# Optimization experiments

Measured on AMD Instinct MI355X. Metric: run time of the kernel, lower is better.

Reference implementation:

```python
import jax, jax.numpy as jnp
import numpy as np

B, C1, C2, H, L, D, NC = 32, 256, 256, 64, 40, 768, 8
SIGMA_W = 0.1
EMB = (D + NC * 2) // 2  # 392


def _conv(x, w, scale, shift, pad):
    # ultralytics-style Conv: conv2d(bias=False) + eval-mode BN (folded into per-channel
    # scale/shift) + SiLU activation
    y = jax.lax.conv_general_dilated(x, w, (1, 1), [(pad, pad), (pad, pad)],
                                     dimension_numbers=('NCHW', 'OIHW', 'NCHW'))
    y = y * scale[None, :, None, None] + shift[None, :, None, None]
    return y * jax.nn.sigmoid(y)  # SiLU


def _l2norm(x, eps=1e-12):
    n = jnp.sqrt(jnp.sum(x * x, axis=1, keepdims=True))
    return x / jnp.maximum(n, eps)


def setup_inputs() -> dict:
    key = jax.random.key(0)
    ks = jax.random.split(key, 20)
    img = jax.random.normal(ks[0], (B, C1, H, H), jnp.float32)
    flang = jax.random.normal(ks[1], (B, L, D), jnp.float32)
    # contiguous valid mask with >=3 tokens (CLS + >=1 word + SEP)
    lens = jax.random.randint(ks[2], (B,), 3, L + 1)
    word_mask = (jnp.arange(L)[None, :] < lens[:, None]).astype(jnp.int32)
    p = lambda k, s: jax.random.normal(k, s, jnp.float32) * 0.02
    return {
        'img': img, 'flang': flang, 'word_mask': word_mask,
        'w_visu': p(ks[3], (C2, C1, 1, 1)), 's_visu': jnp.ones((C2,)), 'b_visu': jnp.zeros((C2,)),
        'w_g': p(ks[4], (NC, NC, 1, 1)), 's_g': jnp.ones((NC,)), 'b_g': jnp.zeros((NC,)),
        'w_b': p(ks[5], (NC, NC, 1, 1)), 's_b': jnp.ones((NC,)), 'b_b': jnp.zeros((NC,)),
        'W1': p(ks[6], (EMB, D)), 'b1': jnp.zeros((EMB,)),
        'W2': p(ks[7], (2 * NC, EMB)), 'b2': jnp.zeros((2 * NC,)),
        'w_f1': p(ks[8], (C1, C1, 1, 1)), 's_f1': jnp.ones((C1,)), 'b_f1': jnp.zeros((C1,)),
        'w_f2': p(ks[9], (C1, C1, 3, 3)), 's_f2': jnp.ones((C1,)), 'b_f2': jnp.zeros((C1,)),
        'w_f3': p(ks[10], (C2, C1, 1, 1)), 'bias_f3': jnp.zeros((C2,)),
        'add_weight': jnp.zeros((), jnp.float32),
    }


def reference(img, flang, word_mask, w_visu, s_visu, b_visu, w_g, s_g, b_g,
              w_b, s_b, b_b, W1, b1, W2, b2, w_f1, s_f1, b_f1, w_f2, s_f2, b_f2,
              w_f3, bias_f3, add_weight):
    height = img.shape[2]
    # mapping_visu: Conv 1x1 + BN + SiLU, then tanh
    map_visu = jnp.tanh(_conv(img, w_visu, s_visu, b_visu, 0))  # [B,C2,H,H]

    # vectorized get_avg_flang: mean over selected tokens excluding first and last selected
    m = word_mask.astype(jnp.int32)
    csum = jnp.cumsum(m, axis=1)                     # [B,L]
    total = csum[:, -1:]
    inner = ((m == 1) & (csum > 1) & (csum < total)).astype(flang.dtype)  # [B,L]
    cnt = jnp.sum(inner, axis=1, keepdims=True)
    flang_avg = jnp.sum(flang * inner[:, :, None], axis=1) / cnt  # [B,D]

    # mapping_lang: two stacked Linears (no activation between), then sigmoid
    h = flang_avg @ W1.T + b1
    map_flang = jax.nn.sigmoid(h @ W2.T + b2)        # [B,2*NC]
    maps = map_flang.reshape(-1, NC, 2)

    sigma = SIGMA_W * height
    yc = (maps[:, :, 0] * height).astype(jnp.int32)[:, :, None, None]
    xc = (maps[:, :, 1] * height).astype(jnp.int32)[:, :, None, None]
    gy, gx = jnp.meshgrid(jnp.arange(height), jnp.arange(height), indexing='ij')
    gy = gy[None, None]; gx = gx[None, None]
    d2 = ((gy - yc) ** 2 + (gx - xc) ** 2).astype(jnp.float32)
    weights = jnp.exp(-d2 / (2.0 * sigma ** 2))      # [B,NC,H,H]

    gamma = jnp.tanh(_conv(weights, w_g, s_g, b_g, 0))
    beta = jnp.tanh(_conv(weights, w_b, s_b, b_b, 0))
    g = jnp.mean(gamma, axis=1, keepdims=True)       # [B,1,H,H]
    b = jnp.max(beta, axis=1, keepdims=True)         # [B,1,H,H]

    v_film = _l2norm(g * map_visu + b)               # [B,C2,H,H]
    # mapping_fusion: Conv1x1 -> Conv3x3 -> plain Conv2d 1x1 with bias
    v = _conv(v_film, w_f1, s_f1, b_f1, 0)
    v = _conv(v, w_f2, s_f2, b_f2, 1)
    v_film = jax.lax.conv_general_dilated(v, w_f3, (1, 1), [(0, 0), (0, 0)],
                                          dimension_numbers=('NCHW', 'OIHW', 'NCHW'))
    v_film = v_film + bias_f3[None, :, None, None]

    add_w = jnp.tanh(add_weight)
    v_add = (1.0 + add_w) * img + (1.0 - add_w) * v_film
    return _l2norm(v_add)
```

## Files before the change

kernel.cpp:

```cpp
#include <hip/hip_runtime.h>
#include <hip/hip_bf16.h>

#define B_   32
#define C_   256
#define HH   64
#define P_   4096
#define L_   40
#define D_   768
#define NC_  8
#define EMB_ 392
#define CP_  (C_*P_)
#define LOS  264

typedef __attribute__((ext_vector_type(8))) short bf16x8;
typedef __attribute__((ext_vector_type(4))) float f32x4;
typedef unsigned short u16;

static __device__ __forceinline__ float siluf(float y) {
    return y / (1.f + expf(-y));
}
static __device__ __forceinline__ u16 f2b(float f) {
    __hip_bfloat16 h = __float2bfloat16(f);
    return *reinterpret_cast<u16*>(&h);
}
static __device__ __forceinline__ float b2f(u16 u) {
    unsigned v = ((unsigned)u) << 16;
    return __int_as_float((int)v);
}

typedef __attribute__((address_space(1))) const unsigned int g_u32;
typedef __attribute__((address_space(3))) unsigned int l_u32;
static __device__ __forceinline__ void gl_lds(const u16* g, short* l) {
    __builtin_amdgcn_global_load_lds((g_u32*)g, (l_u32*)l, 16, 0, 0);
}
#define VMCNT6() asm volatile("s_waitcnt vmcnt(6)" ::: "memory")
#define VMCNT0() asm volatile("s_waitcnt vmcnt(0)" ::: "memory")
#define RBAR()  do { __builtin_amdgcn_s_barrier(); __builtin_amdgcn_sched_barrier(0); } while (0)

__global__ __launch_bounds__(256) void k_prep(
    const float* __restrict__ wv, const float* __restrict__ wf1,
    const float* __restrict__ wf3, const float* __restrict__ wf2,
    u16* __restrict__ WV, u16* __restrict__ WF1,
    u16* __restrict__ WF3, u16* __restrict__ WF2, u16* __restrict__ zblk)
{
    int i = blockIdx.x * 256 + threadIdx.x;
    int oc = i >> 8, ic = i & 255;
    WV[i]  = f2b(wv[i]);
    WF1[i] = f2b(wf1[i]);
    WF3[i] = f2b(wf3[i]);
#pragma unroll
    for (int tap = 0; tap < 9; ++tap)
        WF2[oc * 2304 + tap * 256 + ic] = f2b(wf2[oc * 2304 + ic * 9 + tap]);
    if (blockIdx.x == 0 && threadIdx.x < 16) zblk[threadIdx.x] = 0;
}

__global__ __launch_bounds__(256) void k_imgT(
    const float* __restrict__ img, u16* __restrict__ imgT)
{
    int b = blockIdx.z, pix0 = blockIdx.x * 32, ic0 = blockIdx.y * 32;
    int t = threadIdx.x;
    __shared__ float T[32][33];
    int ic = t >> 3, ps = (t & 7) * 4;
    f32x4 v = *(const f32x4*)&img[((size_t)b * C_ + ic0 + ic) * P_ + pix0 + ps];
    T[ic][ps] = v[0]; T[ic][ps + 1] = v[1]; T[ic][ps + 2] = v[2]; T[ic][ps + 3] = v[3];
    __syncthreads();
    int px = t >> 3, sg = (t & 7) * 4;
    u16 o0 = f2b(T[sg + 0][px]), o1 = f2b(T[sg + 1][px]);
    u16 o2 = f2b(T[sg + 2][px]), o3 = f2b(T[sg + 3][px]);
    uint2 val;
    val.x = (unsigned)o0 | ((unsigned)o1 << 16);
    val.y = (unsigned)o2 | ((unsigned)o3 << 16);
    *(uint2*)(imgT + ((size_t)b * P_ + pix0 + px) * C_ + ic0 + sg) = val;
}

__global__ __launch_bounds__(256) void k_lang(
    const float* __restrict__ flang, const int* __restrict__ wmask,
    const float* __restrict__ W1, const float* __restrict__ b1,
    const float* __restrict__ W2, const float* __restrict__ b2,
    int* __restrict__ centers)
{
    int b = blockIdx.x, tid = threadIdx.x;
    __shared__ float inner[L_];
    __shared__ float cnt_s;
    __shared__ float favg[D_];
    __shared__ float hbuf[EMB_];
    __shared__ float mfs[16];

    if (tid == 0) {
        int total = 0;
        for (int l = 0; l < L_; ++l) total += wmask[b * L_ + l];
        int c = 0, cntv = 0;
        for (int l = 0; l < L_; ++l) {
            int m = wmask[b * L_ + l];
            c += m;
            float f = (m == 1 && c > 1 && c < total) ? 1.f : 0.f;
            inner[l] = f;
            cntv += (f != 0.f);
        }
        cnt_s = (float)cntv;
    }
    __syncthreads();
    float cinv = 1.f / cnt_s;
    for (int d = tid; d < D_; d += 256) {
        float s = 0.f;
        for (int l = 0; l < L_; ++l)
            s += flang[((size_t)b * L_ + l) * D_ + d] * inner[l];
        favg[d] = s * cinv;
    }
    __syncthreads();
    for (int e = tid; e < EMB_; e += 256) {
        float s = b1[e];
        const float* w = W1 + (size_t)e * D_;
        for (int d = 0; d < D_; ++d) s += w[d] * favg[d];
        hbuf[e] = s;
    }
    __syncthreads();
    if (tid < 16) {
        float s = b2[tid];
        const float* w = W2 + tid * EMB_;
        for (int d = 0; d < EMB_; ++d) s += w[d] * hbuf[d];
        mfs[tid] = 1.f / (1.f + expf(-s));
    }
    __syncthreads();
    if (tid < NC_) {
        centers[b * (NC_ * 2) + tid * 2 + 0] = (int)(mfs[tid * 2 + 0] * (float)HH);
        centers[b * (NC_ * 2) + tid * 2 + 1] = (int)(mfs[tid * 2 + 1] * (float)HH);
    }
}

__global__ __launch_bounds__(256) void k_gb(
    const int* __restrict__ centers,
    const float* __restrict__ wg, const float* __restrict__ sg, const float* __restrict__ bg,
    const float* __restrict__ wb, const float* __restrict__ sb, const float* __restrict__ bb,
    float* __restrict__ gmap, float* __restrict__ bmap)
{
    int idx = blockIdx.x * 256 + threadIdx.x;
    int b = idx >> 12;
    int p = idx & 4095;
    int gy = p >> 6, gx = p & 63;

    float w[NC_];
#pragma unroll
    for (int nc = 0; nc < NC_; ++nc) {
        int yc = centers[b * (NC_ * 2) + nc * 2 + 0];
        int xc = centers[b * (NC_ * 2) + nc * 2 + 1];
        int dy = gy - yc, dx = gx - xc;
        w[nc] = expf(-(float)(dy * dy + dx * dx) / 81.92f);
    }
    float gsum = 0.f, bmx = -1e30f;
#pragma unroll
    for (int c = 0; c < NC_; ++c) {
        float ag = 0.f, ab = 0.f;
#pragma unroll
        for (int ic = 0; ic < NC_; ++ic) {
            ag += wg[c * NC_ + ic] * w[ic];
            ab += wb[c * NC_ + ic] * w[ic];
        }
        gsum += tanhf(siluf(sg[c] * ag + bg[c]));
        bmx = fmaxf(bmx, tanhf(siluf(sb[c] * ab + bb[c])));
    }
    gmap[idx] = gsum * (1.f / (float)NC_);
    bmap[idx] = bmx;
}

static __device__ __forceinline__ void frag_load(const short* sA, const short* sW,
                                                 int l15, int qa, int w,
                                                 bf16x8 a[8], bf16x8 bb[4])
{
#pragma unroll
    for (int m = 0; m < 8; ++m)
        a[m] = *(const bf16x8*)&sA[(m * 16 + l15) * 32 + qa * 8];
#pragma unroll
    for (int n = 0; n < 4; ++n)
        bb[n] = *(const bf16x8*)&sW[(w * 64 + n * 16 + l15) * 32 + qa * 8];
}
static __device__ __forceinline__ void frag_compute(const bf16x8 a[8], const bf16x8 bb[4],
                                                    f32x4 acc[8][4])
{
#pragma unroll
    for (int m = 0; m < 8; ++m)
#pragma unroll
        for (int n = 0; n < 4; ++n)
            acc[m][n] = __builtin_amdgcn_mfma_f32_16x16x32_bf16(a[m], bb[n], acc[m][n], 0, 0, 0);
}

__global__ __launch_bounds__(256, 2) void k_visu(
    const u16* __restrict__ X, const u16* __restrict__ W,
    const float* __restrict__ s_visu, const float* __restrict__ b_visu,
    const float* __restrict__ gmap, const float* __restrict__ bmap,
    u16* __restrict__ Y)
{
    int b = blockIdx.y, p0 = blockIdx.x * 128, t = threadIdx.x;
    int lane = t & 63, w = t >> 6;
    int l15 = t & 15, q = (t >> 4) & 3;
    int qa = q ^ ((l15 >> 1) & 3);
    int lc = (lane & 3) ^ ((lane >> 3) & 3);
    int lp = lane >> 2;
    __shared__ __align__(16) short SM[128 * LOS];
    __shared__ float red[4][128];
    __shared__ float invs[128];
    const u16* Xb = X + (size_t)b * CP_;

    f32x4 acc[8][4];
#pragma unroll
    for (int m = 0; m < 8; ++m)
#pragma unroll
        for (int n = 0; n < 4; ++n) acc[m][n] = (f32x4)0.f;

    auto stage = [&](int s, int buf) {
        int k0 = s * 32;
        short* bA = SM + buf * 12288;
        short* bW = bA + 4096;
#pragma unroll
        for (int i = 0; i < 2; ++i) {
            int pr = (w * 2 + i) * 16 + lp;
            gl_lds(Xb + (size_t)(p0 + pr) * C_ + k0 + lc * 8, bA + (w * 2 + i) * 512);
        }
#pragma unroll
        for (int j = 0; j < 4; ++j) {
            int oc = (w * 4 + j) * 16 + lp;
            gl_lds(W + (size_t)oc * 256 + k0 + lc * 8, bW + (w * 4 + j) * 512);
        }
    };

    stage(0, 0);
    VMCNT0();
    __syncthreads();
    for (int s = 0; s < 8; ++s) {
        int cur = s & 1;
        bf16x8 a[8], bb[4];
        frag_load(SM + cur * 12288, SM + cur * 12288 + 4096, l15, qa, w, a, bb);
        if (s < 7) stage(s + 1, cur ^ 1);
        frag_compute(a, bb, acc);
        VMCNT0();
        __syncthreads();
    }

    float sc[4], sh[4];
#pragma unroll
    for (int n = 0; n < 4; ++n) {
        int oc = w * 64 + n * 16 + l15;
        sc[n] = s_visu[oc]; sh[n] = b_visu[oc];
    }
    short* LO = SM;
#pragma unroll
    for (int m = 0; m < 8; ++m) {
        f32x4 gv = *(const f32x4*)&gmap[(size_t)b * P_ + p0 + m * 16 + q * 4];
        f32x4 bm = *(const f32x4*)&bmap[(size_t)b * P_ + p0 + m * 16 + q * 4];
        float ps[4] = {0.f, 0.f, 0.f, 0.f};
#pragma unroll
        for (int n = 0; n < 4; ++n)
#pragma unroll
            for (int r = 0; r < 4; ++r) {
                float y = sc[n] * acc[m][n][r] + sh[n];
                float v = gv[r] * tanhf(siluf(y)) + bm[r];
                ps[r] += v * v;
                LO[(m * 16 + q * 4 + r) * LOS + w * 64 + n * 16 + l15] = (short)f2b(v);
            }
#pragma unroll
        for (int r = 0; r < 4; ++r) {
            float p = ps[r];
            p += __shfl_xor(p, 1);
            p += __shfl_xor(p, 2);
            p += __shfl_xor(p, 4);
            p += __shfl_xor(p, 8);
            if (l15 == 0) red[w][m * 16 + q * 4 + r] = p;
        }
    }
    __syncthreads();
    if (t < 128) {
        float s = red[0][t] + red[1][t] + red[2][t] + red[3][t];
        invs[t] = 1.f / fmaxf(sqrtf(s), 1e-12f);
    }
    __syncthreads();

    u16* Yb = Y + (size_t)b * CP_ + (size_t)p0 * C_;
#pragma unroll
    for (int h = 0; h < 2; ++h) {
        int row = h * 64 + (t >> 2);
        float inv = invs[row];
        const short* sp = &LO[row * LOS];
        u16* dp = Yb + (size_t)row * C_;
#pragma unroll
        for (int u = 0; u < 8; ++u) {
            int c = (t & 3) * 8 + u * 32;
            uint4 vv = *(const uint4*)(sp + c);
            const u16* e = (const u16*)&vv;
            uint4 o;
            u16* oe = (u16*)&o;
#pragma unroll
            for (int k = 0; k < 8; ++k) oe[k] = f2b(b2f(e[k]) * inv);
            *(uint4*)(dp + c) = o;
        }
    }
}

__global__ __launch_bounds__(256, 2) void k_f1(
    const u16* __restrict__ X, const u16* __restrict__ W,
    const float* __restrict__ scale, const float* __restrict__ shift,
    u16* __restrict__ Y)
{
    int b = blockIdx.y, p0 = blockIdx.x * 128, t = threadIdx.x;
    int lane = t & 63, w = t >> 6;
    int l15 = t & 15, q = (t >> 4) & 3;
    int qa = q ^ ((l15 >> 1) & 3);
    int lc = (lane & 3) ^ ((lane >> 3) & 3);
    int lp = lane >> 2;
    __shared__ __align__(16) short SM[128 * LOS];
    const u16* Xb = X + (size_t)b * CP_;

    f32x4 acc[8][4];
#pragma unroll
    for (int m = 0; m < 8; ++m)
#pragma unroll
        for (int n = 0; n < 4; ++n) acc[m][n] = (f32x4)0.f;

    auto stage = [&](int s, int buf) {
        int k0 = s * 32;
        short* bA = SM + buf * 12288;
        short* bW = bA + 4096;
#pragma unroll
        for (int i = 0; i < 2; ++i) {
            int pr = (w * 2 + i) * 16 + lp;
            gl_lds(Xb + (size_t)(p0 + pr) * C_ + k0 + lc * 8, bA + (w * 2 + i) * 512);
        }
#pragma unroll
        for (int j = 0; j < 4; ++j) {
            int oc = (w * 4 + j) * 16 + lp;
            gl_lds(W + (size_t)oc * 256 + k0 + lc * 8, bW + (w * 4 + j) * 512);
        }
    };

    stage(0, 0);
    VMCNT0();
    __syncthreads();
    for (int s = 0; s < 8; ++s) {
        int cur = s & 1;
        bf16x8 a[8], bb[4];
        frag_load(SM + cur * 12288, SM + cur * 12288 + 4096, l15, qa, w, a, bb);
        if (s < 7) stage(s + 1, cur ^ 1);
        frag_compute(a, bb, acc);
        VMCNT0();
        __syncthreads();
    }

    float sc[4], sh[4];
#pragma unroll
    for (int n = 0; n < 4; ++n) {
        int oc = w * 64 + n * 16 + l15;
        sc[n] = scale[oc]; sh[n] = shift[oc];
    }
    short* LO = SM;
#pragma unroll
    for (int m = 0; m < 8; ++m)
#pragma unroll
        for (int n = 0; n < 4; ++n)
#pragma unroll
            for (int r = 0; r < 4; ++r) {
                float v = siluf(sc[n] * acc[m][n][r] + sh[n]);
                LO[(m * 16 + q * 4 + r) * LOS + w * 64 + n * 16 + l15] = (short)f2b(v);
            }
    __syncthreads();

    u16* Yb = Y + (size_t)b * CP_ + (size_t)p0 * C_;
#pragma unroll
    for (int h = 0; h < 2; ++h) {
        int row = h * 64 + (t >> 2);
        const short* sp = &LO[row * LOS];
        u16* dp = Yb + (size_t)row * C_;
#pragma unroll
        for (int u = 0; u < 8; ++u) {
            int c = (t & 3) * 8 + u * 32;
            *(uint4*)(dp + c) = *(const uint4*)(sp + c);
        }
    }
}

__global__ __launch_bounds__(256, 2) void k_f2(
    const u16* __restrict__ X, const u16* __restrict__ W,
    const float* __restrict__ scale, const float* __restrict__ shift,
    const u16* __restrict__ zblk, u16* __restrict__ Y)
{
    int b = blockIdx.y, p0 = blockIdx.x * 128, t = threadIdx.x;
    int lane = t & 63, w = t >> 6;
    int l15 = t & 15, q = (t >> 4) & 3;
    int qa = q ^ ((l15 >> 1) & 3);
    int lc = (lane & 3) ^ ((lane >> 3) & 3);
    int lp = lane >> 2;
    __shared__ __align__(16) short SM[3 * 12288];
    const u16* Xb = X + (size_t)b * CP_;

    f32x4 acc[8][4];
#pragma unroll
    for (int m = 0; m < 8; ++m)
#pragma unroll
        for (int n = 0; n < 4; ++n) acc[m][n] = (f32x4)0.f;

    auto stage = [&](int s, int buf) {
        int k0 = s * 32;
        int tap = s >> 3;
        int icb = (s & 7) * 32;
        int dy = tap / 3 - 1, dx = tap - (tap / 3) * 3 - 1;
        short* bA = SM + buf * 12288;
        short* bW = bA + 4096;
#pragma unroll
        for (int i = 0; i < 2; ++i) {
            int pr = (w * 2 + i) * 16 + lp;
            int p = p0 + pr;
            int y = (p >> 6) + dy, x = (p & 63) + dx;
            const u16* gp = ((unsigned)y < (unsigned)HH && (unsigned)x < (unsigned)HH)
                ? Xb + (size_t)(y * HH + x) * C_ + icb + lc * 8
                : zblk;
            gl_lds(gp, bA + (w * 2 + i) * 512);
        }
#pragma unroll
        for (int j = 0; j < 4; ++j) {
            int oc = (w * 4 + j) * 16 + lp;
            gl_lds(W + (size_t)oc * 2304 + k0 + lc * 8, bW + (w * 4 + j) * 512);
        }
    };

    stage(0, 0);
    stage(1, 1);
    VMCNT6();
    RBAR();
    for (int s = 0; s < 72; ++s) {
        int cur = s % 3;
        bf16x8 a[8], bb[4];
        frag_load(SM + cur * 12288, SM + cur * 12288 + 4096, l15, qa, w, a, bb);
        if (s < 70) stage(s + 2, (s + 2) % 3);
        frag_compute(a, bb, acc);
        if (s < 70) { VMCNT6(); } else { VMCNT0(); }
        RBAR();
    }

    float sc[4], sh[4];
#pragma unroll
    for (int n = 0; n < 4; ++n) {
        int oc = w * 64 + n * 16 + l15;
        sc[n] = scale[oc]; sh[n] = shift[oc];
    }
    short* LO = SM;
#pragma unroll
    for (int m = 0; m < 8; ++m)
#pragma unroll
        for (int n = 0; n < 4; ++n)
#pragma unroll
            for (int r = 0; r < 4; ++r) {
                float v = siluf(sc[n] * acc[m][n][r] + sh[n]);
                LO[(m * 16 + q * 4 + r) * LOS + w * 64 + n * 16 + l15] = (short)f2b(v);
            }
    __syncthreads();

    u16* Yb = Y + (size_t)b * CP_ + (size_t)p0 * C_;
#pragma unroll
    for (int h = 0; h < 2; ++h) {
        int row = h * 64 + (t >> 2);
        const short* sp = &LO[row * LOS];
        u16* dp = Yb + (size_t)row * C_;
#pragma unroll
        for (int u = 0; u < 8; ++u) {
            int c = (t & 3) * 8 + u * 32;
            *(uint4*)(dp + c) = *(const uint4*)(sp + c);
        }
    }
}

__global__ __launch_bounds__(256, 2) void k_final(
    const u16* __restrict__ X, const u16* __restrict__ W,
    const float* __restrict__ bias_f3, const float* __restrict__ img,
    const float* __restrict__ add_w, float* __restrict__ out)
{
    int b = blockIdx.y, p0 = blockIdx.x * 128, t = threadIdx.x;
    int lane = t & 63, w = t >> 6;
    int l15 = t & 15, q = (t >> 4) & 3;
    int qa = q ^ ((l15 >> 1) & 3);
    int lc = (lane & 3) ^ ((lane >> 3) & 3);
    int lp = lane >> 2;
    __shared__ __align__(16) short SM[2 * 12288];
    __shared__ float red[4][128];
    __shared__ float invs[128];
    const u16* Xb = X + (size_t)b * CP_;

    f32x4 acc[8][4];
#pragma unroll
    for (int m = 0; m < 8; ++m)
#pragma unroll
        for (int n = 0; n < 4; ++n) acc[m][n] = (f32x4)0.f;

    auto stage = [&](int s, int buf) {
        int k0 = s * 32;
        short* bA = SM + buf * 12288;
        short* bW = bA + 4096;
#pragma unroll
        for (int i = 0; i < 2; ++i) {
            int pr = (w * 2 + i) * 16 + lp;
            gl_lds(Xb + (size_t)(p0 + pr) * C_ + k0 + lc * 8, bA + (w * 2 + i) * 512);
        }
#pragma unroll
        for (int j = 0; j < 4; ++j) {
            int oc = (w * 4 + j) * 16 + lp;
            gl_lds(W + (size_t)oc * 256 + k0 + lc * 8, bW + (w * 4 + j) * 512);
        }
    };

    stage(0, 0);
    VMCNT0();
    __syncthreads();
    for (int s = 0; s < 8; ++s) {
        int cur = s & 1;
        bf16x8 a[8], bb[4];
        frag_load(SM + cur * 12288, SM + cur * 12288 + 4096, l15, qa, w, a, bb);
        if (s < 7) stage(s + 1, cur ^ 1);
        frag_compute(a, bb, acc);
        VMCNT0();
        __syncthreads();
    }

    float aw = tanhf(add_w[0]);
    float c1 = 1.f + aw, c2 = 1.f - aw;
    float bf[4];
#pragma unroll
    for (int n = 0; n < 4; ++n) bf[n] = bias_f3[w * 64 + n * 16 + l15];

#pragma unroll
    for (int m = 0; m < 8; ++m) {
        float ps[4] = {0.f, 0.f, 0.f, 0.f};
#pragma unroll
        for (int n = 0; n < 4; ++n) {
            int oc = w * 64 + n * 16 + l15;
            f32x4 iv = *(const f32x4*)&img[((size_t)b * C_ + oc) * P_ + p0 + m * 16 + q * 4];
#pragma unroll
            for (int r = 0; r < 4; ++r) {
                float v = c1 * iv[r] + c2 * (acc[m][n][r] + bf[n]);
                acc[m][n][r] = v;
                ps[r] += v * v;
            }
        }
#pragma unroll
        for (int r = 0; r < 4; ++r) {
            float p = ps[r];
            p += __shfl_xor(p, 1);
            p += __shfl_xor(p, 2);
            p += __shfl_xor(p, 4);
            p += __shfl_xor(p, 8);
            if (l15 == 0) red[w][m * 16 + q * 4 + r] = p;
        }
    }
    __syncthreads();
    if (t < 128) {
        float s = red[0][t] + red[1][t] + red[2][t] + red[3][t];
        invs[t] = 1.f / fmaxf(sqrtf(s), 1e-12f);
    }
    __syncthreads();
#pragma unroll
    for (int m = 0; m < 8; ++m) {
        f32x4 iv = *(const f32x4*)&invs[m * 16 + q * 4];
#pragma unroll
        for (int n = 0; n < 4; ++n) {
            int oc = w * 64 + n * 16 + l15;
            f32x4 o;
#pragma unroll
            for (int r = 0; r < 4; ++r) o[r] = acc[m][n][r] * iv[r];
            *(f32x4*)&out[((size_t)b * C_ + oc) * P_ + p0 + m * 16 + q * 4] = o;
        }
    }
}

extern "C" void kernel_launch(void* const* d_in, const int* in_sizes, int n_in,
                              void* d_out, int out_size, void* d_ws, size_t ws_size,
                              hipStream_t stream)
{
    const float* img     = (const float*)d_in[0];
    const float* flang   = (const float*)d_in[1];
    const int*   wmask   = (const int*)d_in[2];
    const float* w_visu  = (const float*)d_in[3];
    const float* s_visu  = (const float*)d_in[4];
    const float* b_visu  = (const float*)d_in[5];
    const float* w_g     = (const float*)d_in[6];
    const float* s_g     = (const float*)d_in[7];
    const float* b_g     = (const float*)d_in[8];
    const float* w_b     = (const float*)d_in[9];
    const float* s_b     = (const float*)d_in[10];
    const float* b_b     = (const float*)d_in[11];
    const float* W1      = (const float*)d_in[12];
    const float* b1      = (const float*)d_in[13];
    const float* W2      = (const float*)d_in[14];
    const float* b2      = (const float*)d_in[15];
    const float* w_f1    = (const float*)d_in[16];
    const float* s_f1    = (const float*)d_in[17];
    const float* b_f1    = (const float*)d_in[18];
    const float* w_f2    = (const float*)d_in[19];
    const float* s_f2    = (const float*)d_in[20];
    const float* b_f2    = (const float*)d_in[21];
    const float* w_f3    = (const float*)d_in[22];
    const float* bias_f3 = (const float*)d_in[23];
    const float* add_w   = (const float*)d_in[24];

    float* out = (float*)d_out;

    u16* bigA = (u16*)d_ws;
    u16* bigB = bigA + (size_t)B_ * CP_;
    u16* WV   = bigB + (size_t)B_ * CP_;
    u16* WF1  = WV + 65536;
    u16* WF3  = WF1 + 65536;
    u16* WF2  = WF3 + 65536;
    float* gmap = (float*)(WF2 + 589824);
    float* bmap = gmap + (size_t)B_ * P_;
    int* centers = (int*)(bmap + (size_t)B_ * P_);
    u16* zblk = (u16*)(centers + 512);

    k_prep<<<256, 256, 0, stream>>>(w_visu, w_f1, w_f3, w_f2, WV, WF1, WF3, WF2, zblk);
    k_lang<<<B_, 256, 0, stream>>>(flang, wmask, W1, b1, W2, b2, centers);
    k_gb<<<(B_ * P_) / 256, 256, 0, stream>>>(centers, w_g, s_g, b_g, w_b, s_b, b_b, gmap, bmap);
    k_imgT<<<dim3(P_ / 32, C_ / 32, B_), 256, 0, stream>>>(img, bigB);
    k_visu<<<dim3(P_ / 128, B_), 256, 0, stream>>>(bigB, WV, s_visu, b_visu, gmap, bmap, bigA);
    k_f1<<<dim3(P_ / 128, B_), 256, 0, stream>>>(bigA, WF1, s_f1, b_f1, bigB);
    k_f2<<<dim3(P_ / 128, B_), 256, 0, stream>>>(bigB, WF2, s_f2, b_f2, zblk, bigA);
    k_final<<<dim3(P_ / 128, B_), 256, 0, stream>>>(bigA, WF3, bias_f3, img, add_w, out);
}
```

Baseline: 490.3 us.

## Fuse visual mapping conv and first fusion 1x1 conv into one kernel

Merges the visual 1x1 conv (with FiLM modulation and L2 normalisation) and the following 1x1 fusion conv into a single kernel. The normalised tile stays in a swizzled shared-memory buffer and feeds the second GEMM directly, with only the weights streamed. This removes one full bf16 activation write and read through global memory plus a kernel launch. The trade-off is that the second GEMM loads its weights without double buffering, adding a global-load wait each k-step. Output is written in place over the input buffer, which is safe because each block reads only its own rows.

```diff
diff --git a/kernel.cpp b/kernel.cpp
--- a/kernel.cpp
+++ b/kernel.cpp
@@ -27,6 +27,10 @@
     unsigned v = ((unsigned)u) << 16;
     return __int_as_float((int)v);
 }
+static __device__ __forceinline__ int swz(int row, int col) {
+    int ch = (col >> 3) ^ ((row & 7) << 2);
+    return row * 256 + ch * 8 + (col & 7);
+}
 
 typedef __attribute__((address_space(1))) const unsigned int g_u32;
 typedef __attribute__((address_space(3))) unsigned int l_u32;
@@ -184,10 +188,11 @@
             acc[m][n] = __builtin_amdgcn_mfma_f32_16x16x32_bf16(a[m], bb[n], acc[m][n], 0, 0, 0);
 }
 
-__global__ __launch_bounds__(256, 2) void k_visu(
-    const u16* __restrict__ X, const u16* __restrict__ W,
+__global__ __launch_bounds__(256, 2) void k_vf1(
+    const u16* __restrict__ X, const u16* __restrict__ WV, const u16* __restrict__ WF1,
     const float* __restrict__ s_visu, const float* __restrict__ b_visu,
     const float* __restrict__ gmap, const float* __restrict__ bmap,
+    const float* __restrict__ s_f1, const float* __restrict__ b_f1,
     u16* __restrict__ Y)
 {
     int b = blockIdx.y, p0 = blockIdx.x * 128, t = threadIdx.x;
@@ -196,9 +201,10 @@
     int qa = q ^ ((l15 >> 1) & 3);
     int lc = (lane & 3) ^ ((lane >> 3) & 3);
     int lp = lane >> 2;
-    __shared__ __align__(16) short SM[128 * LOS];
-    __shared__ float red[4][128];
-    __shared__ float invs[128];
+    __shared__ __align__(16) short LO[32768];
+    __shared__ __align__(16) short W2[8192];
+    float* red  = (float*)W2;
+    float* invs = (float*)(W2 + 1024);
     const u16* Xb = X + (size_t)b * CP_;
 
     f32x4 acc[8][4];
@@ -207,9 +213,9 @@
 #pragma unroll
         for (int n = 0; n < 4; ++n) acc[m][n] = (f32x4)0.f;
 
-    auto stage = [&](int s, int buf) {
+    auto stage1 = [&](int s, int buf) {
         int k0 = s * 32;
-        short* bA = SM + buf * 12288;
+        short* bA = LO + buf * 12288;
         short* bW = bA + 4096;
 #pragma unroll
         for (int i = 0; i < 2; ++i) {
@@ -219,159 +225,132 @@
 #pragma unroll
         for (int j = 0; j < 4; ++j) {
             int oc = (w * 4 + j) * 16 + lp;
-            gl_lds(W + (size_t)oc * 256 + k0 + lc * 8, bW + (w * 4 + j) * 512);
+            gl_lds(WV + (size_t)oc * 256 + k0 + lc * 8, bW + (w * 4 + j) * 512);
         }
     };
-
-    stage(0, 0);
+    stage1(0, 0);
     VMCNT0();
     __syncthreads();
     for (int s = 0; s < 8; ++s) {
         int cur = s & 1;
         bf16x8 a[8], bb[4];
-        frag_load(SM + cur * 12288, SM + cur * 12288 + 4096, l15, qa, w, a, bb);
-        if (s < 7) stage(s + 1, cur ^ 1);
+        frag_load(LO + cur * 12288, LO + cur * 12288 + 4096, l15, qa, w, a, bb);
+        if (s < 7) stage1(s + 1, cur ^ 1);
         frag_compute(a, bb, acc);
         VMCNT0();
         __syncthreads();
     }
 
-    float sc[4], sh[4];
-#pragma unroll
-    for (int n = 0; n < 4; ++n) {
-        int oc = w * 64 + n * 16 + l15;
-        sc[n] = s_visu[oc]; sh[n] = b_visu[oc];
-    }
-    short* LO = SM;
+    {
+        float sc[4], sh[4];
+#pragma unroll
+        for (int n = 0; n < 4; ++n) {
+            int oc = w * 64 + n * 16 + l15;
+            sc[n] = s_visu[oc]; sh[n] = b_visu[oc];
+        }
+#pragma unroll
+        for (int m = 0; m < 8; ++m) {
+            f32x4 gv = *(const f32x4*)&gmap[(size_t)b * P_ + p0 + m * 16 + q * 4];
+            f32x4 bm = *(const f32x4*)&bmap[(size_t)b * P_ + p0 + m * 16 + q * 4];
+            float ps[4] = {0.f, 0.f, 0.f, 0.f};
+#pragma unroll
+            for (int n = 0; n < 4; ++n)
+#pragma unroll
+                for (int r = 0; r < 4; ++r) {
+                    float y = sc[n] * acc[m][n][r] + sh[n];
+                    float v = gv[r] * tanhf(siluf(y)) + bm[r];
+                    acc[m][n][r] = v;
+                    ps[r] += v * v;
+                }
+#pragma unroll
+            for (int r = 0; r < 4; ++r) {
+                float p = ps[r];
+                p += __shfl_xor(p, 1);
+                p += __shfl_xor(p, 2);
+                p += __shfl_xor(p, 4);
+                p += __shfl_xor(p, 8);
+                if (l15 == 0) red[w * 128 + m * 16 + q * 4 + r] = p;
+            }
+        }
+    }
+    __syncthreads();
+    if (t < 128) {
+        float s = red[0 * 128 + t] + red[1 * 128 + t] + red[2 * 128 + t] + red[3 * 128 + t];
+        invs[t] = 1.f / fmaxf(sqrtf(s), 1e-12f);
+    }
+    __syncthreads();
+
 #pragma unroll
     for (int m = 0; m < 8; ++m) {
-        f32x4 gv = *(const f32x4*)&gmap[(size_t)b * P_ + p0 + m * 16 + q * 4];
-        f32x4 bm = *(const f32x4*)&bmap[(size_t)b * P_ + p0 + m * 16 + q * 4];
-        float ps[4] = {0.f, 0.f, 0.f, 0.f};
+        f32x4 iv = *(const f32x4*)&invs[m * 16 + q * 4];
 #pragma unroll
         for (int n = 0; n < 4; ++n)
 #pragma unroll
             for (int r = 0; r < 4; ++r) {
-                float y = sc[n] * acc[m][n][r] + sh[n];
-                float v = gv[r] * tanhf(siluf(y)) + bm[r];
-                ps[r] += v * v;
-                LO[(m * 16 + q * 4 + r) * LOS + w * 64 + n * 16 + l15] = (short)f2b(v);
+                int row = m * 16 + q * 4 + r;
+                int col = w * 64 + n * 16 + l15;
+                LO[swz(row, col)] = (short)f2b(acc[m][n][r] * iv[r]);
             }
-#pragma unroll
-        for (int r = 0; r < 4; ++r) {
-            float p = ps[r];
-            p += __shfl_xor(p, 1);
-            p += __shfl_xor(p, 2);
-            p += __shfl_xor(p, 4);
-            p += __shfl_xor(p, 8);
-            if (l15 == 0) red[w][m * 16 + q * 4 + r] = p;
-        }
-    }
-    __syncthreads();
-    if (t < 128) {
-        float s = red[0][t] + red[1][t] + red[2][t] + red[3][t];
-        invs[t] = 1.f / fmaxf(sqrtf(s), 1e-12f);
-    }
-    __syncthreads();
-
+    }
+    __syncthreads();
+
+#pragma unroll
+    for (int m = 0; m < 8; ++m)
+#pragma unroll
+        for (int n = 0; n < 4; ++n) acc[m][n] = (f32x4)0.f;
+
+    for (int ks = 0; ks < 8; ++ks) {
+#pragma unroll
+        for (int j = 0; j < 4; ++j) {
+            int oc = (w * 4 + j) * 16 + lp;
+            gl_lds(WF1 + (size_t)oc * 256 + ks * 32 + lc * 8, W2 + (w * 4 + j) * 512);
+        }
+        VMCNT0();
+        __syncthreads();
+        bf16x8 a[8], bb[4];
+#pragma unroll
+        for (int m = 0; m < 8; ++m) {
+            int row = m * 16 + l15;
+            int ch = (ks * 4 + q) ^ ((row & 7) << 2);
+            a[m] = *(const bf16x8*)&LO[row * 256 + ch * 8];
+        }
+#pragma unroll
+        for (int n = 0; n < 4; ++n)
+            bb[n] = *(const bf16x8*)&W2[(w * 64 + n * 16 + l15) * 32 + qa * 8];
+        frag_compute(a, bb, acc);
+        __syncthreads();
+    }
+
+    {
+        float sc[4], sh[4];
+#pragma unroll
+        for (int n = 0; n < 4; ++n) {
+            int oc = w * 64 + n * 16 + l15;
+            sc[n] = s_f1[oc]; sh[n] = b_f1[oc];
+        }
+        __syncthreads();
+#pragma unroll
+        for (int m = 0; m < 8; ++m)
+#pragma unroll
+            for (int n = 0; n < 4; ++n)
+#pragma unroll
+                for (int r = 0; r < 4; ++r) {
+                    int row = m * 16 + q * 4 + r;
+                    int col = w * 64 + n * 16 + l15;
+                    LO[swz(row, col)] = (short)f2b(siluf(sc[n] * acc[m][n][r] + sh[n]));
+                }
+    }
+    __syncthreads();
     u16* Yb = Y + (size_t)b * CP_ + (size_t)p0 * C_;
 #pragma unroll
     for (int h = 0; h < 2; ++h) {
         int row = h * 64 + (t >> 2);
-        float inv = invs[row];
-        const short* sp = &LO[row * LOS];
         u16* dp = Yb + (size_t)row * C_;
 #pragma unroll
         for (int u = 0; u < 8; ++u) {
-            int c = (t & 3) * 8 + u * 32;
-            uint4 vv = *(const uint4*)(sp + c);
-            const u16* e = (const u16*)&vv;
-            uint4 o;
-            u16* oe = (u16*)&o;
-#pragma unroll
-            for (int k = 0; k < 8; ++k) oe[k] = f2b(b2f(e[k]) * inv);
-            *(uint4*)(dp + c) = o;
-        }
-    }
-}
-
-__global__ __launch_bounds__(256, 2) void k_f1(
-    const u16* __restrict__ X, const u16* __restrict__ W,
-    const float* __restrict__ scale, const float* __restrict__ shift,
-    u16* __restrict__ Y)
-{
-    int b = blockIdx.y, p0 = blockIdx.x * 128, t = threadIdx.x;
-    int lane = t & 63, w = t >> 6;
-    int l15 = t & 15, q = (t >> 4) & 3;
-    int qa = q ^ ((l15 >> 1) & 3);
-    int lc = (lane & 3) ^ ((lane >> 3) & 3);
-    int lp = lane >> 2;
-    __shared__ __align__(16) short SM[128 * LOS];
-    const u16* Xb = X + (size_t)b * CP_;
-
-    f32x4 acc[8][4];
-#pragma unroll
-    for (int m = 0; m < 8; ++m)
-#pragma unroll
-        for (int n = 0; n < 4; ++n) acc[m][n] = (f32x4)0.f;
-
-    auto stage = [&](int s, int buf) {
-        int k0 = s * 32;
-        short* bA = SM + buf * 12288;
-        short* bW = bA + 4096;
-#pragma unroll
-        for (int i = 0; i < 2; ++i) {
-            int pr = (w * 2 + i) * 16 + lp;
-            gl_lds(Xb + (size_t)(p0 + pr) * C_ + k0 + lc * 8, bA + (w * 2 + i) * 512);
-        }
-#pragma unroll
-        for (int j = 0; j < 4; ++j) {
-            int oc = (w * 4 + j) * 16 + lp;
-            gl_lds(W + (size_t)oc * 256 + k0 + lc * 8, bW + (w * 4 + j) * 512);
-        }
-    };
-
-    stage(0, 0);
-    VMCNT0();
-    __syncthreads();
-    for (int s = 0; s < 8; ++s) {
-        int cur = s & 1;
-        bf16x8 a[8], bb[4];
-        frag_load(SM + cur * 12288, SM + cur * 12288 + 4096, l15, qa, w, a, bb);
-        if (s < 7) stage(s + 1, cur ^ 1);
-        frag_compute(a, bb, acc);
-        VMCNT0();
-        __syncthreads();
-    }
-
-    float sc[4], sh[4];
-#pragma unroll
-    for (int n = 0; n < 4; ++n) {
-        int oc = w * 64 + n * 16 + l15;
-        sc[n] = scale[oc]; sh[n] = shift[oc];
-    }
-    short* LO = SM;
-#pragma unroll
-    for (int m = 0; m < 8; ++m)
-#pragma unroll
-        for (int n = 0; n < 4; ++n)
-#pragma unroll
-            for (int r = 0; r < 4; ++r) {
-                float v = siluf(sc[n] * acc[m][n][r] + sh[n]);
-                LO[(m * 16 + q * 4 + r) * LOS + w * 64 + n * 16 + l15] = (short)f2b(v);
-            }
-    __syncthreads();
-
-    u16* Yb = Y + (size_t)b * CP_ + (size_t)p0 * C_;
-#pragma unroll
-    for (int h = 0; h < 2; ++h) {
-        int row = h * 64 + (t >> 2);
-        const short* sp = &LO[row * LOS];
-        u16* dp = Yb + (size_t)row * C_;
-#pragma unroll
-        for (int u = 0; u < 8; ++u) {
-            int c = (t & 3) * 8 + u * 32;
-            *(uint4*)(dp + c) = *(const uint4*)(sp + c);
+            int ch = (t & 3) + u * 4;
+            int sc_ = ch ^ ((row & 7) << 2);
+            *(uint4*)(dp + ch * 8) = *(const uint4*)&LO[row * 256 + sc_ * 8];
         }
     }
 }
@@ -614,8 +593,8 @@
     k_lang<<<B_, 256, 0, stream>>>(flang, wmask, W1, b1, W2, b2, centers);
     k_gb<<<(B_ * P_) / 256, 256, 0, stream>>>(centers, w_g, s_g, b_g, w_b, s_b, b_b, gmap, bmap);
     k_imgT<<<dim3(P_ / 32, C_ / 32, B_), 256, 0, stream>>>(img, bigB);
-    k_visu<<<dim3(P_ / 128, B_), 256, 0, stream>>>(bigB, WV, s_visu, b_visu, gmap, bmap, bigA);
-    k_f1<<<dim3(P_ / 128, B_), 256, 0, stream>>>(bigA, WF1, s_f1, b_f1, bigB);
+    k_vf1<<<dim3(P_ / 128, B_), 256, 0, stream>>>(bigB, WV, WF1, s_visu, b_visu,
+                                                  gmap, bmap, s_f1, b_f1, bigB);
     k_f2<<<dim3(P_ / 128, B_), 256, 0, stream>>>(bigB, WF2, s_f2, b_f2, zblk, bigA);
     k_final<<<dim3(P_ / 128, B_), 256, 0, stream>>>(bigA, WF3, bias_f3, img, add_w, out);
 }
```

After: 507.9 us. +3.6%, slower.

## Split 3x3 conv kernel output channels into two 128-wide tiles

Applied to the files above, without the earlier changes.

The 3x3 fusion conv kernel now tiles output channels in halves, giving each block 128 pixels by 128 output channels and launching twice as many blocks. Accumulators and the per-stage LDS footprint shrink, which allows three blocks per CU instead of two for more occupancy and latency hiding. The cost is that each activation tile is now loaded twice from global memory (once per channel half), and arithmetic intensity per block goes down.

```diff
diff --git a/kernel.cpp b/kernel.cpp
--- a/kernel.cpp
+++ b/kernel.cpp
@@ -11,6 +11,7 @@
 #define EMB_ 392
 #define CP_  (C_*P_)
 #define LOS  264
+#define LOS2 136
 
 typedef __attribute__((ext_vector_type(8))) short bf16x8;
 typedef __attribute__((ext_vector_type(4))) float f32x4;
@@ -33,7 +34,7 @@
 static __device__ __forceinline__ void gl_lds(const u16* g, short* l) {
     __builtin_amdgcn_global_load_lds((g_u32*)g, (l_u32*)l, 16, 0, 0);
 }
-#define VMCNT6() asm volatile("s_waitcnt vmcnt(6)" ::: "memory")
+#define VMCNT4() asm volatile("s_waitcnt vmcnt(4)" ::: "memory")
 #define VMCNT0() asm volatile("s_waitcnt vmcnt(0)" ::: "memory")
 #define RBAR()  do { __builtin_amdgcn_s_barrier(); __builtin_amdgcn_sched_barrier(0); } while (0)
 
@@ -376,32 +377,33 @@
     }
 }
 
-__global__ __launch_bounds__(256, 2) void k_f2(
+__global__ __launch_bounds__(256, 3) void k_f2(
     const u16* __restrict__ X, const u16* __restrict__ W,
     const float* __restrict__ scale, const float* __restrict__ shift,
     const u16* __restrict__ zblk, u16* __restrict__ Y)
 {
-    int b = blockIdx.y, p0 = blockIdx.x * 128, t = threadIdx.x;
+    int b = blockIdx.z, p0 = blockIdx.x * 128, oc0 = blockIdx.y * 128;
+    int t = threadIdx.x;
     int lane = t & 63, w = t >> 6;
     int l15 = t & 15, q = (t >> 4) & 3;
     int qa = q ^ ((l15 >> 1) & 3);
     int lc = (lane & 3) ^ ((lane >> 3) & 3);
     int lp = lane >> 2;
-    __shared__ __align__(16) short SM[3 * 12288];
+    __shared__ __align__(16) short SM[3 * 8192];
     const u16* Xb = X + (size_t)b * CP_;
 
-    f32x4 acc[8][4];
-#pragma unroll
-    for (int m = 0; m < 8; ++m)
-#pragma unroll
-        for (int n = 0; n < 4; ++n) acc[m][n] = (f32x4)0.f;
+    f32x4 acc[8][2];
+#pragma unroll
+    for (int m = 0; m < 8; ++m)
+#pragma unroll
+        for (int n = 0; n < 2; ++n) acc[m][n] = (f32x4)0.f;
 
     auto stage = [&](int s, int buf) {
         int k0 = s * 32;
         int tap = s >> 3;
         int icb = (s & 7) * 32;
         int dy = tap / 3 - 1, dx = tap - (tap / 3) * 3 - 1;
-        short* bA = SM + buf * 12288;
+        short* bA = SM + buf * 8192;
         short* bW = bA + 4096;
 #pragma unroll
         for (int i = 0; i < 2; ++i) {
@@ -414,55 +416,63 @@
             gl_lds(gp, bA + (w * 2 + i) * 512);
         }
 #pragma unroll
-        for (int j = 0; j < 4; ++j) {
-            int oc = (w * 4 + j) * 16 + lp;
-            gl_lds(W + (size_t)oc * 2304 + k0 + lc * 8, bW + (w * 4 + j) * 512);
+        for (int j = 0; j < 2; ++j) {
+            int oc = (w * 2 + j) * 16 + lp;
+            gl_lds(W + (size_t)(oc0 + oc) * 2304 + k0 + lc * 8, bW + (w * 2 + j) * 512);
         }
     };
 
     stage(0, 0);
     stage(1, 1);
-    VMCNT6();
+    VMCNT4();
     RBAR();
     for (int s = 0; s < 72; ++s) {
         int cur = s % 3;
-        bf16x8 a[8], bb[4];
-        frag_load(SM + cur * 12288, SM + cur * 12288 + 4096, l15, qa, w, a, bb);
+        const short* bA = SM + cur * 8192;
+        const short* bW = bA + 4096;
+        bf16x8 a[8], bb[2];
+#pragma unroll
+        for (int m = 0; m < 8; ++m)
+            a[m] = *(const bf16x8*)&bA[(m * 16 + l15) * 32 + qa * 8];
+#pragma unroll
+        for (int n = 0; n < 2; ++n)
+            bb[n] = *(const bf16x8*)&bW[(w * 32 + n * 16 + l15) * 32 + qa * 8];
         if (s < 70) stage(s + 2, (s + 2) % 3);
-        frag_compute(a, bb, acc);
-        if (s < 70) { VMCNT6(); } else { VMCNT0(); }
+#pragma unroll
+        for (int m = 0; m < 8; ++m)
+#pragma unroll
+            for (int n = 0; n < 2; ++n)
+                acc[m][n] = __builtin_amdgcn_mfma_f32_16x16x32_bf16(a[m], bb[n], acc[m][n], 0, 0, 0);
+        if (s < 70) { VMCNT4(); } else { VMCNT0(); }
         RBAR();
     }
 
-    float sc[4], sh[4];
-#pragma unroll
-    for (int n = 0; n < 4; ++n) {
-        int oc = w * 64 + n * 16 + l15;
+    float sc[2], sh[2];
+#pragma unroll
+    for (int n = 0; n < 2; ++n) {
+        int oc = oc0 + w * 32 + n * 16 + l15;
         sc[n] = scale[oc]; sh[n] = shift[oc];
     }
     short* LO = SM;
 #pragma unroll
     for (int m = 0; m < 8; ++m)
 #pragma unroll
-        for (int n = 0; n < 4; ++n)
+        for (int n = 0; n < 2; ++n)
 #pragma unroll
             for (int r = 0; r < 4; ++r) {
                 float v = siluf(sc[n] * acc[m][n][r] + sh[n]);
-                LO[(m * 16 + q * 4 + r) * LOS + w * 64 + n * 16 + l15] = (short)f2b(v);
+                LO[(m * 16 + q * 4 + r) * LOS2 + w * 32 + n * 16 + l15] = (short)f2b(v);
             }
     __syncthreads();
 
-    u16* Yb = Y + (size_t)b * CP_ + (size_t)p0 * C_;
-#pragma unroll
-    for (int h = 0; h < 2; ++h) {
-        int row = h * 64 + (t >> 2);
-        const short* sp = &LO[row * LOS];
-        u16* dp = Yb + (size_t)row * C_;
-#pragma unroll
-        for (int u = 0; u < 8; ++u) {
-            int c = (t & 3) * 8 + u * 32;
-            *(uint4*)(dp + c) = *(const uint4*)(sp + c);
-        }
+    u16* Yb = Y + (size_t)b * CP_ + (size_t)p0 * C_ + oc0;
+    {
+        int row = t >> 1, cb = (t & 1) * 64;
+        const short* sp = &LO[row * LOS2 + cb];
+        u16* dp = Yb + (size_t)row * C_ + cb;
+#pragma unroll
+        for (int u = 0; u < 8; ++u)
+            *(uint4*)(dp + u * 8) = *(const uint4*)(sp + u * 8);
     }
 }
 
@@ -616,6 +626,6 @@
     k_imgT<<<dim3(P_ / 32, C_ / 32, B_), 256, 0, stream>>>(img, bigB);
     k_visu<<<dim3(P_ / 128, B_), 256, 0, stream>>>(bigB, WV, s_visu, b_visu, gmap, bmap, bigA);
     k_f1<<<dim3(P_ / 128, B_), 256, 0, stream>>>(bigA, WF1, s_f1, b_f1, bigB);
-    k_f2<<<dim3(P_ / 128, B_), 256, 0, stream>>>(bigB, WF2, s_f2, b_f2, zblk, bigA);
+    k_f2<<<dim3(P_ / 128, 2, B_), 256, 0, stream>>>(bigB, WF2, s_f2, b_f2, zblk, bigA);
     k_final<<<dim3(P_ / 128, B_), 256, 0, stream>>>(bigA, WF3, bias_f3, img, add_w, out);
 }
```

Result: slower. 519.6 us (+6.0%).
